# Performance work log

Hardware: AMD Instinct MI355X
Metric: run time of the kernel (lower is better)

The kernel has to match this reference:

```python
import jax, jax.numpy as jnp
import numpy as np

N_NODES = 100000
N_EDGES = 3200000
IN_CH = 128
HID = 64
OUT_CH = 2
BN_EPS = 1e-5


def setup_inputs() -> dict:
    key = jax.random.key(0)
    ks = jax.random.split(key, 16)
    def glorot(k, shape):
        fan_in, fan_out = shape[0], shape[1]
        lim = jnp.sqrt(6.0 / (fan_in + fan_out))
        return jax.random.uniform(k, shape, jnp.float32, -lim, lim)
    inp = {
        "x": jax.random.normal(ks[0], (N_NODES, IN_CH), jnp.float32),
        "edge_index": jax.random.randint(ks[1], (2, N_EDGES), 0, N_NODES, jnp.int64),
        # input projection + input BN
        "Wp": glorot(ks[2], (IN_CH, HID)),
        "bp": jnp.zeros((HID,), jnp.float32),
        "g_in": jnp.ones((HID,), jnp.float32),
        "b_in": jnp.zeros((HID,), jnp.float32),
        # SAGEConv layer 0: lin_l (aggr, with bias) + lin_r (self, no bias)
        "Wl0": glorot(ks[3], (HID, HID)),
        "bl0": jnp.zeros((HID,), jnp.float32),
        "Wr0": glorot(ks[4], (HID, HID)),
        "g0": jnp.ones((HID,), jnp.float32),
        "b0": jnp.zeros((HID,), jnp.float32),
        # SAGEConv layer 1
        "Wl1": glorot(ks[5], (HID, HID)),
        "bl1": jnp.zeros((HID,), jnp.float32),
        "Wr1": glorot(ks[6], (HID, HID)),
        "g1": jnp.ones((HID,), jnp.float32),
        "b1": jnp.zeros((HID,), jnp.float32),
        # output head
        "Wo": glorot(ks[7], (HID, OUT_CH)),
        "bo": jnp.zeros((OUT_CH,), jnp.float32),
    }
    return inp


def _bn(h, g, b):
    # training-mode batchnorm over node dim (biased variance, as torch)
    m = h.mean(axis=0)
    v = h.var(axis=0)
    return g * (h - m) * jax.lax.rsqrt(v + BN_EPS) + b


def _sage_conv(h, src, dst, Wl, bl, Wr):
    # mean aggregation of source features at destination nodes
    msg = h[src]                                              # [E, HID]
    summed = jax.ops.segment_sum(msg, dst, num_segments=N_NODES)
    cnt = jax.ops.segment_sum(jnp.ones((src.shape[0],), h.dtype), dst,
                              num_segments=N_NODES)
    aggr = summed / jnp.maximum(cnt, 1.0)[:, None]
    return aggr @ Wl + bl + h @ Wr


def reference(x, edge_index, Wp, bp, g_in, b_in,
              Wl0, bl0, Wr0, g0, b0,
              Wl1, bl1, Wr1, g1, b1,
              Wo, bo):
    src, dst = edge_index[0], edge_index[1]
    h = jax.nn.relu(_bn(x @ Wp + bp, g_in, b_in))   # dropout: eval no-op
    h_prev = h
    # layer 0 (i=0: no residual)
    h_new = jax.nn.relu(_bn(_sage_conv(h, src, dst, Wl0, bl0, Wr0), g0, b0))
    h_prev, h = h, h_new
    # layer 1 (i=1: residual with h_prev)
    h_new = jax.nn.relu(_bn(_sage_conv(h, src, dst, Wl1, bl1, Wr1), g1, b1))
    h_new = h_new + h_prev
    h = h_new
    return h @ Wo + bo
```

## Files before the change

### kernel.cpp

```cpp
#include <hip/hip_runtime.h>
#include <hip/hip_bf16.h>

#define NN 100000
#define NE 3200000
#define IC 128
#define HD 64
#define BN_EPS 1e-5f
#define NBUK 196
#define MSB 16
#define CAP 20480

__device__ __forceinline__ float bf2f(unsigned short u) {
  return __uint_as_float(((unsigned)u) << 16);
}
__device__ __forceinline__ unsigned int f2bf(float f) {
  unsigned int u = __float_as_uint(f);
  return (u + 0x7FFFu + ((u >> 16) & 1u)) >> 16;
}
__device__ __forceinline__ unsigned int pack2(float a, float b) {
  return f2bf(a) | (f2bf(b) << 16);
}

__global__ __launch_bounds__(256) void k_gemm_in(
    const float* __restrict__ x, const float* __restrict__ Wp,
    const float* __restrict__ bp, unsigned int* __restrict__ pre16,
    float* __restrict__ stats) {
  __shared__ float sW[IC * HD];
  __shared__ unsigned int sXu[64 * 68];
  __shared__ float sStS[256], sStQ[256];
  int tid = threadIdx.x;
  for (int i = tid; i < IC * HD / 4; i += 256)
    *(float4*)&sW[i * 4] = *(const float4*)&Wp[i * 4];
  int cg = tid & 15, rg = tid >> 4;
  int c0 = cg * 4;
  float4 bpc = *(const float4*)&bp[c0];
  float S[4] = {0.f, 0.f, 0.f, 0.f}, Q[4] = {0.f, 0.f, 0.f, 0.f};
  const int NT = (NN + 63) / 64;
  for (int t = blockIdx.x; t < NT; t += gridDim.x) {
    int row0 = t * 64;
    __syncthreads();
    for (int i = tid; i < 1024; i += 256) {
      int r = i >> 4, k8 = i & 15;
      int grow = row0 + r;
      if (grow >= NN) grow = NN - 1;
      const float* xs = &x[(size_t)grow * IC + k8 * 8];
      float4 f0 = *(const float4*)xs;
      float4 f1 = *(const float4*)(xs + 4);
      uint4 p;
      p.x = pack2(f0.x, f0.y);
      p.y = pack2(f0.z, f0.w);
      p.z = pack2(f1.x, f1.y);
      p.w = pack2(f1.z, f1.w);
      *(uint4*)&sXu[r * 68 + k8 * 4] = p;
    }
    __syncthreads();
    float acc[4][4];
#pragma unroll
    for (int r = 0; r < 4; ++r)
#pragma unroll
      for (int c = 0; c < 4; ++c) acc[r][c] = ((const float*)&bpc)[c];
    for (int kg = 0; kg < IC; kg += 4) {
      uint2 xu[4];
      float4 wv[4];
#pragma unroll
      for (int r = 0; r < 4; ++r)
        xu[r] = *(const uint2*)&sXu[(rg * 4 + r) * 68 + (kg >> 1)];
#pragma unroll
      for (int j = 0; j < 4; ++j)
        wv[j] = *(const float4*)&sW[(kg + j) * HD + c0];
#pragma unroll
      for (int r = 0; r < 4; ++r) {
        float xv[4];
        xv[0] = __uint_as_float(xu[r].x << 16);
        xv[1] = __uint_as_float(xu[r].x & 0xFFFF0000u);
        xv[2] = __uint_as_float(xu[r].y << 16);
        xv[3] = __uint_as_float(xu[r].y & 0xFFFF0000u);
#pragma unroll
        for (int j = 0; j < 4; ++j) {
#pragma unroll
          for (int c = 0; c < 4; ++c)
            acc[r][c] = fmaf(xv[j], ((const float*)&wv[j])[c], acc[r][c]);
        }
      }
    }
#pragma unroll
    for (int r = 0; r < 4; ++r) {
      int row = row0 + rg * 4 + r;
      if (row < NN) {
        uint2 o;
        o.x = pack2(acc[r][0], acc[r][1]);
        o.y = pack2(acc[r][2], acc[r][3]);
        *(uint2*)&pre16[(size_t)row * 32 + cg * 2] = o;
#pragma unroll
        for (int c = 0; c < 4; ++c) {
          S[c] += acc[r][c];
          Q[c] = fmaf(acc[r][c], acc[r][c], Q[c]);
        }
      }
    }
  }
#pragma unroll
  for (int c = 0; c < 4; ++c) {
    S[c] += __shfl_xor(S[c], 16);
    S[c] += __shfl_xor(S[c], 32);
    Q[c] += __shfl_xor(Q[c], 16);
    Q[c] += __shfl_xor(Q[c], 32);
  }
  int wave = tid >> 6, lane = tid & 63;
  if (lane < 16) {
#pragma unroll
    for (int c = 0; c < 4; ++c) {
      sStS[wave * 64 + lane * 4 + c] = S[c];
      sStQ[wave * 64 + lane * 4 + c] = Q[c];
    }
  }
  __syncthreads();
  if (tid < 64) {
    float Ts = sStS[tid] + sStS[64 + tid] + sStS[128 + tid] + sStS[192 + tid];
    float Tq = sStQ[tid] + sStQ[64 + tid] + sStQ[128 + tid] + sStQ[192 + tid];
    atomicAdd(&stats[tid], Ts);
    atomicAdd(&stats[64 + tid], Tq);
  }
}

__global__ __launch_bounds__(256) void k_bn_relu(
    const unsigned int* __restrict__ pre16, const float* __restrict__ stats,
    const float* __restrict__ g, const float* __restrict__ b,
    unsigned int* __restrict__ h16u) {
  size_t i = (size_t)blockIdx.x * 256 + threadIdx.x;
  int c0 = ((int)(i & 15)) * 4;
  const float invN = 1.0f / NN;
  uint2 p = *(const uint2*)&pre16[i * 2];
  float v[4];
  v[0] = __uint_as_float(p.x << 16);
  v[1] = __uint_as_float(p.x & 0xFFFF0000u);
  v[2] = __uint_as_float(p.y << 16);
  v[3] = __uint_as_float(p.y & 0xFFFF0000u);
#pragma unroll
  for (int c = 0; c < 4; ++c) {
    float m = stats[c0 + c] * invN;
    float var = stats[64 + c0 + c] * invN - m * m;
    float sc = g[c0 + c] * rsqrtf(var + BN_EPS);
    v[c] = fmaxf((v[c] - m) * sc + b[c0 + c], 0.f);
  }
  uint2 o;
  o.x = pack2(v[0], v[1]);
  o.y = pack2(v[2], v[3]);
  *(uint2*)&h16u[i * 2] = o;
}

__global__ __launch_bounds__(256) void k_initcur(unsigned int* __restrict__ gcur) {
  int t = threadIdx.x;
  if (t < NBUK) gcur[t] = (unsigned int)(t * CAP);
}

__global__ __launch_bounds__(256) void k_msplit(
    const int* __restrict__ src, const int* __restrict__ dst,
    unsigned int* __restrict__ gcur, unsigned int* __restrict__ staging) {
  __shared__ unsigned int hist[NBUK];
  __shared__ unsigned int gbase[NBUK];
  int tid = threadIdx.x;
  for (int i = tid; i < NBUK; i += 256) hist[i] = 0u;
  __syncthreads();
  int e0 = blockIdx.x * (256 * MSB);
  unsigned int pk[MSB], rk[MSB], bk[MSB];
#pragma unroll
  for (int i = 0; i < MSB; ++i) {
    int e = e0 + i * 256 + tid;
    if (e < NE) {
      int d = dst[e];
      unsigned int b = (unsigned int)(d >> 9);
      rk[i] = atomicAdd(&hist[b], 1u);
      pk[i] = (unsigned int)src[e] | ((unsigned int)(d & 511) << 17);
      bk[i] = b;
    } else {
      bk[i] = 0xFFFFFFFFu;
    }
  }
  __syncthreads();
  for (int i = tid; i < NBUK; i += 256)
    if (hist[i]) gbase[i] = atomicAdd(&gcur[i], hist[i]);
  __syncthreads();
#pragma unroll
  for (int i = 0; i < MSB; ++i)
    if (bk[i] != 0xFFFFFFFFu) staging[gbase[bk[i]] + rk[i]] = pk[i];
}

__global__ __launch_bounds__(256) void k_cscan(
    const unsigned int* __restrict__ gcur, unsigned int* __restrict__ gstart) {
  __shared__ unsigned int s[256];
  int t = threadIdx.x;
  unsigned int my = (t < NBUK) ? (gcur[t] - (unsigned int)(t * CAP)) : 0u;
  s[t] = my;
  __syncthreads();
  for (int off = 1; off < 256; off <<= 1) {
    unsigned int v = (t >= off) ? s[t - off] : 0u;
    __syncthreads();
    s[t] += v;
    __syncthreads();
  }
  if (t < NBUK) gstart[t] = s[t] - my;
  if (t == NBUK - 1) gstart[NBUK] = s[t];
}

__global__ __launch_bounds__(512) void k_bucket_sort(
    const unsigned int* __restrict__ staging,
    const unsigned int* __restrict__ gstart, unsigned int* __restrict__ nstart,
    unsigned int* __restrict__ srcoff) {
  __shared__ unsigned int hist[512];
  __shared__ unsigned int sc[512];
  __shared__ unsigned int cur[512];
  int b = blockIdx.x, t = threadIdx.x;
  hist[t] = 0u;
  __syncthreads();
  int base_in = b * CAP;
  int lo = (int)gstart[b];
  int cnt = (int)gstart[b + 1] - lo;
  for (int i = t; i < cnt; i += 512)
    atomicAdd(&hist[staging[base_in + i] >> 17], 1u);
  __syncthreads();
  unsigned int my = hist[t];
  sc[t] = my;
  __syncthreads();
  for (int off = 1; off < 512; off <<= 1) {
    unsigned int v = (t >= off) ? sc[t - off] : 0u;
    __syncthreads();
    sc[t] += v;
    __syncthreads();
  }
  unsigned int st = (unsigned int)lo + sc[t] - my;
  cur[t] = st;
  int node = b * 512 + t;
  if (node < NN) {
    nstart[node] = st;
    if (node == NN - 1) nstart[NN] = st + my;
  }
  __syncthreads();
  for (int i = t; i < cnt; i += 512) {
    unsigned int u = staging[base_in + i];
    unsigned int pos = atomicAdd(&cur[u >> 17], 1u);
    srcoff[pos] = (u & 0x1FFFFu) << 7;
  }
}

__global__ __launch_bounds__(256) void k_aggr_sorted(
    const unsigned int* __restrict__ srcoff,
    const unsigned int* __restrict__ nstart,
    const unsigned short* __restrict__ h16,
    unsigned short* __restrict__ a16) {
  int lane = threadIdx.x & 63;
  int n = (int)((blockIdx.x * 256 + threadIdx.x) >> 6);
  if (n >= NN) return;
  int g = lane >> 3;
  int q = lane & 7;
  int e0 = (int)nstart[n];
  int e1 = (int)nstart[n + 1];
  const char* hbase = (const char*)h16 + q * 16;
  float a0 = 0.f, a1 = 0.f, a2 = 0.f, a3 = 0.f;
  float a4 = 0.f, a5 = 0.f, a6 = 0.f, a7 = 0.f;
  float b0 = 0.f, b1 = 0.f, b2 = 0.f, b3 = 0.f;
  float b4 = 0.f, b5 = 0.f, b6 = 0.f, b7 = 0.f;
  int e = e0 + g;
  for (; e + 8 < e1; e += 16) {
    unsigned int o0 = srcoff[e];
    unsigned int o1 = srcoff[e + 8];
    uint4 u0 = *(const uint4*)(hbase + o0);
    uint4 u1 = *(const uint4*)(hbase + o1);
    a0 += __uint_as_float(u0.x << 16);
    a1 += __uint_as_float(u0.x & 0xFFFF0000u);
    a2 += __uint_as_float(u0.y << 16);
    a3 += __uint_as_float(u0.y & 0xFFFF0000u);
    a4 += __uint_as_float(u0.z << 16);
    a5 += __uint_as_float(u0.z & 0xFFFF0000u);
    a6 += __uint_as_float(u0.w << 16);
    a7 += __uint_as_float(u0.w & 0xFFFF0000u);
    b0 += __uint_as_float(u1.x << 16);
    b1 += __uint_as_float(u1.x & 0xFFFF0000u);
    b2 += __uint_as_float(u1.y << 16);
    b3 += __uint_as_float(u1.y & 0xFFFF0000u);
    b4 += __uint_as_float(u1.z << 16);
    b5 += __uint_as_float(u1.z & 0xFFFF0000u);
    b6 += __uint_as_float(u1.w << 16);
    b7 += __uint_as_float(u1.w & 0xFFFF0000u);
  }
  if (e < e1) {
    unsigned int o0 = srcoff[e];
    uint4 u0 = *(const uint4*)(hbase + o0);
    a0 += __uint_as_float(u0.x << 16);
    a1 += __uint_as_float(u0.x & 0xFFFF0000u);
    a2 += __uint_as_float(u0.y << 16);
    a3 += __uint_as_float(u0.y & 0xFFFF0000u);
    a4 += __uint_as_float(u0.z << 16);
    a5 += __uint_as_float(u0.z & 0xFFFF0000u);
    a6 += __uint_as_float(u0.w << 16);
    a7 += __uint_as_float(u0.w & 0xFFFF0000u);
  }
  a0 += b0; a1 += b1; a2 += b2; a3 += b3;
  a4 += b4; a5 += b5; a6 += b6; a7 += b7;
#pragma unroll
  for (int off = 8; off <= 32; off <<= 1) {
    a0 += __shfl_xor(a0, off);
    a1 += __shfl_xor(a1, off);
    a2 += __shfl_xor(a2, off);
    a3 += __shfl_xor(a3, off);
    a4 += __shfl_xor(a4, off);
    a5 += __shfl_xor(a5, off);
    a6 += __shfl_xor(a6, off);
    a7 += __shfl_xor(a7, off);
  }
  if (g == 0) {
    float cntf = (float)(e1 - e0);
    float inv = (cntf > 0.f) ? 1.0f / cntf : 0.f;
    uint4 o;
    o.x = pack2(a0 * inv, a1 * inv);
    o.y = pack2(a2 * inv, a3 * inv);
    o.z = pack2(a4 * inv, a5 * inv);
    o.w = pack2(a6 * inv, a7 * inv);
    *(uint4*)((char*)a16 + (size_t)n * 128 + q * 16) = o;
  }
}

__global__ __launch_bounds__(256) void k_combine(
    const unsigned int* __restrict__ a16u,
    const unsigned int* __restrict__ h16u, const float* __restrict__ Wl,
    const float* __restrict__ bl, const float* __restrict__ Wr,
    unsigned int* __restrict__ pre16, float* __restrict__ stats) {
  __shared__ float sWl[HD * HD], sWr[HD * HD];
  __shared__ unsigned int sAu[64 * 36], sHu[64 * 36];
  __shared__ float sStS[256], sStQ[256];
  int tid = threadIdx.x;
  for (int i = tid; i < HD * HD / 4; i += 256) {
    *(float4*)&sWl[i * 4] = *(const float4*)&Wl[i * 4];
    *(float4*)&sWr[i * 4] = *(const float4*)&Wr[i * 4];
  }
  int cg = tid & 15, rg = tid >> 4;
  int c0 = cg * 4;
  float4 blc = *(const float4*)&bl[c0];
  float S[4] = {0.f, 0.f, 0.f, 0.f}, Q[4] = {0.f, 0.f, 0.f, 0.f};
  const int NT = (NN + 63) / 64;
  for (int t = blockIdx.x; t < NT; t += gridDim.x) {
    int row0 = t * 64;
    __syncthreads();
    for (int i = tid; i < 512; i += 256) {
      int r = i >> 3, c4 = i & 7;
      int grow = row0 + r;
      if (grow >= NN) grow = NN - 1;
      *(uint4*)&sAu[r * 36 + c4 * 4] =
          *(const uint4*)&a16u[(size_t)grow * 32 + c4 * 4];
      *(uint4*)&sHu[r * 36 + c4 * 4] =
          *(const uint4*)&h16u[(size_t)grow * 32 + c4 * 4];
    }
    __syncthreads();
    float acc[4][4];
#pragma unroll
    for (int r = 0; r < 4; ++r)
#pragma unroll
      for (int c = 0; c < 4; ++c) acc[r][c] = ((const float*)&blc)[c];
    for (int kg = 0; kg < HD; kg += 4) {
      uint2 au[4], hu[4];
      float4 wlv[4], wrv[4];
#pragma unroll
      for (int r = 0; r < 4; ++r) {
        au[r] = *(const uint2*)&sAu[(rg * 4 + r) * 36 + (kg >> 1)];
        hu[r] = *(const uint2*)&sHu[(rg * 4 + r) * 36 + (kg >> 1)];
      }
#pragma unroll
      for (int j = 0; j < 4; ++j) {
        wlv[j] = *(const float4*)&sWl[(kg + j) * HD + c0];
        wrv[j] = *(const float4*)&sWr[(kg + j) * HD + c0];
      }
#pragma unroll
      for (int r = 0; r < 4; ++r) {
        float av[4], hv[4];
        av[0] = __uint_as_float(au[r].x << 16);
        av[1] = __uint_as_float(au[r].x & 0xFFFF0000u);
        av[2] = __uint_as_float(au[r].y << 16);
        av[3] = __uint_as_float(au[r].y & 0xFFFF0000u);
        hv[0] = __uint_as_float(hu[r].x << 16);
        hv[1] = __uint_as_float(hu[r].x & 0xFFFF0000u);
        hv[2] = __uint_as_float(hu[r].y << 16);
        hv[3] = __uint_as_float(hu[r].y & 0xFFFF0000u);
#pragma unroll
        for (int j = 0; j < 4; ++j) {
#pragma unroll
          for (int c = 0; c < 4; ++c) {
            acc[r][c] = fmaf(av[j], ((const float*)&wlv[j])[c], acc[r][c]);
            acc[r][c] = fmaf(hv[j], ((const float*)&wrv[j])[c], acc[r][c]);
          }
        }
      }
    }
#pragma unroll
    for (int r = 0; r < 4; ++r) {
      int row = row0 + rg * 4 + r;
      if (row < NN) {
        uint2 o;
        o.x = pack2(acc[r][0], acc[r][1]);
        o.y = pack2(acc[r][2], acc[r][3]);
        *(uint2*)&pre16[(size_t)row * 32 + cg * 2] = o;
#pragma unroll
        for (int c = 0; c < 4; ++c) {
          S[c] += acc[r][c];
          Q[c] = fmaf(acc[r][c], acc[r][c], Q[c]);
        }
      }
    }
  }
#pragma unroll
  for (int c = 0; c < 4; ++c) {
    S[c] += __shfl_xor(S[c], 16);
    S[c] += __shfl_xor(S[c], 32);
    Q[c] += __shfl_xor(Q[c], 16);
    Q[c] += __shfl_xor(Q[c], 32);
  }
  int wave = tid >> 6, lane = tid & 63;
  if (lane < 16) {
#pragma unroll
    for (int c = 0; c < 4; ++c) {
      sStS[wave * 64 + lane * 4 + c] = S[c];
      sStQ[wave * 64 + lane * 4 + c] = Q[c];
    }
  }
  __syncthreads();
  if (tid < 64) {
    float Ts = sStS[tid] + sStS[64 + tid] + sStS[128 + tid] + sStS[192 + tid];
    float Tq = sStQ[tid] + sStQ[64 + tid] + sStQ[128 + tid] + sStQ[192 + tid];
    atomicAdd(&stats[tid], Ts);
    atomicAdd(&stats[64 + tid], Tq);
  }
}

__global__ __launch_bounds__(256) void k_bn_relu_head(
    const unsigned short* __restrict__ pre16,
    const float* __restrict__ stats, const float* __restrict__ g,
    const float* __restrict__ b, const unsigned short* __restrict__ resid16,
    const float* __restrict__ Wo, const float* __restrict__ bo,
    float* __restrict__ out) {
  int lane = threadIdx.x & 63;
  int wid = (int)((blockIdx.x * blockDim.x + threadIdx.x) >> 6);
  int nw = (int)((gridDim.x * blockDim.x) >> 6);
  const float invN = 1.0f / NN;
  float m = stats[lane] * invN;
  float v = stats[64 + lane] * invN - m * m;
  float sc = g[lane] * rsqrtf(v + BN_EPS);
  float bb = b[lane];
  float w0 = Wo[lane * 2], w1 = Wo[lane * 2 + 1];
  float b0 = bo[0], b1 = bo[1];
  for (int row = wid; row < NN; row += nw) {
    size_t i = (size_t)row * HD + lane;
    float val = (bf2f(pre16[i]) - m) * sc + bb;
    val = fmaxf(val, 0.f) + bf2f(resid16[i]);
    float a0 = val * w0, a1 = val * w1;
#pragma unroll
    for (int off = 32; off > 0; off >>= 1) {
      a0 += __shfl_down(a0, off);
      a1 += __shfl_down(a1, off);
    }
    if (lane == 0) {
      out[(size_t)row * 2] = a0 + b0;
      out[(size_t)row * 2 + 1] = a1 + b1;
    }
  }
}

extern "C" void kernel_launch(void* const* d_in, const int* in_sizes, int n_in,
                              void* d_out, int out_size, void* d_ws,
                              size_t ws_size, hipStream_t stream) {
  const float* x = (const float*)d_in[0];
  const int* ei = (const int*)d_in[1];
  const float* Wp = (const float*)d_in[2];
  const float* bp = (const float*)d_in[3];
  const float* g_in = (const float*)d_in[4];
  const float* b_in = (const float*)d_in[5];
  const float* Wl0 = (const float*)d_in[6];
  const float* bl0 = (const float*)d_in[7];
  const float* Wr0 = (const float*)d_in[8];
  const float* g0 = (const float*)d_in[9];
  const float* b0 = (const float*)d_in[10];
  const float* Wl1 = (const float*)d_in[11];
  const float* bl1 = (const float*)d_in[12];
  const float* Wr1 = (const float*)d_in[13];
  const float* g1 = (const float*)d_in[14];
  const float* b1 = (const float*)d_in[15];
  const float* Wo = (const float*)d_in[16];
  const float* bo = (const float*)d_in[17];
  float* out = (float*)d_out;

  const int* src = ei;
  const int* dst = ei + NE;

  unsigned int* pre16 = (unsigned int*)d_ws;
  unsigned short* h0 = (unsigned short*)(pre16 + (size_t)NN * 32);
  unsigned short* h1 = h0 + (size_t)NN * HD;
  unsigned short* a16 = h1 + (size_t)NN * HD;
  unsigned int* staging = (unsigned int*)(a16 + (size_t)NN * HD);
  unsigned int* srcoff = staging + (size_t)NBUK * CAP;
  unsigned int* nstart = srcoff + NE;
  unsigned int* gstart = nstart + NN + 1;
  unsigned int* gcur = gstart + NBUK + 1;
  float* stats0 = (float*)(gcur + NBUK);
  float* stats1 = stats0 + 128;
  float* stats2 = stats1 + 128;

  const int BNR_BLOCKS = (NN * HD / 4) / 256;
  const int AGGR_BLOCKS = 25000;
  const int MS_BLOCKS = (NE + 256 * MSB - 1) / (256 * MSB);

  hipMemsetAsync(stats0, 0, 3 * 128 * sizeof(float), stream);

  k_gemm_in<<<768, 256, 0, stream>>>(x, Wp, bp, pre16, stats0);
  k_bn_relu<<<BNR_BLOCKS, 256, 0, stream>>>(pre16, stats0, g_in, b_in,
                                            (unsigned int*)h0);

  k_initcur<<<1, 256, 0, stream>>>(gcur);
  k_msplit<<<MS_BLOCKS, 256, 0, stream>>>(src, dst, gcur, staging);
  k_cscan<<<1, 256, 0, stream>>>(gcur, gstart);
  k_bucket_sort<<<NBUK, 512, 0, stream>>>(staging, gstart, nstart, srcoff);

  k_aggr_sorted<<<AGGR_BLOCKS, 256, 0, stream>>>(srcoff, nstart, h0, a16);
  k_combine<<<768, 256, 0, stream>>>((const unsigned int*)a16,
                                     (const unsigned int*)h0, Wl0, bl0, Wr0,
                                     pre16, stats1);
  k_bn_relu<<<BNR_BLOCKS, 256, 0, stream>>>(pre16, stats1, g0, b0,
                                            (unsigned int*)h1);

  k_aggr_sorted<<<AGGR_BLOCKS, 256, 0, stream>>>(srcoff, nstart, h1, a16);
  k_combine<<<768, 256, 0, stream>>>((const unsigned int*)a16,
                                     (const unsigned int*)h1, Wl1, bl1, Wr1,
                                     pre16, stats2);
  k_bn_relu_head<<<1024, 256, 0, stream>>>((const unsigned short*)pre16,
                                           stats2, g1, b1, h0, Wo, bo, out);
}
```

Baseline: 360.4 us.

## Use bf16 MFMA instructions for input projection and SAGE combine GEMMs

Replaces the scalar FMA register-tiled GEMMs in the input projection and the two combine kernels with 16x16x32 bf16 MFMA intrinsics. Weights are pre-packed into bf16 fragments in shared memory, and out-of-range rows are zero-filled instead of clamped. The aim is to cut the ALU cost of the dense matmuls. In exchange, output stores become scattered 2-byte writes per lane instead of packed 8-byte writes, and weights are now rounded to bf16, which loses some precision.

```diff
diff --git a/kernel.cpp b/kernel.cpp
--- a/kernel.cpp
+++ b/kernel.cpp
@@ -10,6 +10,9 @@
 #define MSB 16
 #define CAP 20480
 
+typedef __attribute__((ext_vector_type(8))) short bf16x8;
+typedef __attribute__((ext_vector_type(4))) float f32x4;
+
 __device__ __forceinline__ float bf2f(unsigned short u) {
   return __uint_as_float(((unsigned)u) << 16);
 }
@@ -23,17 +26,27 @@
 
 __global__ __launch_bounds__(256) void k_gemm_in(
     const float* __restrict__ x, const float* __restrict__ Wp,
-    const float* __restrict__ bp, unsigned int* __restrict__ pre16,
+    const float* __restrict__ bp, unsigned short* __restrict__ pre16,
     float* __restrict__ stats) {
-  __shared__ float sW[IC * HD];
   __shared__ unsigned int sXu[64 * 68];
+  __shared__ uint4 sWb[16 * 64];
   __shared__ float sStS[256], sStQ[256];
   int tid = threadIdx.x;
-  for (int i = tid; i < IC * HD / 4; i += 256)
-    *(float4*)&sW[i * 4] = *(const float4*)&Wp[i * 4];
-  int cg = tid & 15, rg = tid >> 4;
-  int c0 = cg * 4;
-  float4 bpc = *(const float4*)&bp[c0];
+  int wave = tid >> 6, lane = tid & 63;
+  int lm = lane & 15, lb = lane >> 4;
+  for (int i = tid; i < 1024; i += 256) {
+    int b = i >> 6, n = i & 63;
+    const float* wp = &Wp[(size_t)(8 * b) * HD + n];
+    uint4 p;
+    p.x = pack2(wp[0], wp[HD]);
+    p.y = pack2(wp[2 * HD], wp[3 * HD]);
+    p.z = pack2(wp[4 * HD], wp[5 * HD]);
+    p.w = pack2(wp[6 * HD], wp[7 * HD]);
+    sWb[i] = p;
+  }
+  float bias[4];
+#pragma unroll
+  for (int nt = 0; nt < 4; ++nt) bias[nt] = bp[nt * 16 + lm];
   float S[4] = {0.f, 0.f, 0.f, 0.f}, Q[4] = {0.f, 0.f, 0.f, 0.f};
   const int NT = (NN + 63) / 64;
   for (int t = blockIdx.x; t < NT; t += gridDim.x) {
@@ -42,76 +55,63 @@
     for (int i = tid; i < 1024; i += 256) {
       int r = i >> 4, k8 = i & 15;
       int grow = row0 + r;
-      if (grow >= NN) grow = NN - 1;
-      const float* xs = &x[(size_t)grow * IC + k8 * 8];
-      float4 f0 = *(const float4*)xs;
-      float4 f1 = *(const float4*)(xs + 4);
       uint4 p;
-      p.x = pack2(f0.x, f0.y);
-      p.y = pack2(f0.z, f0.w);
-      p.z = pack2(f1.x, f1.y);
-      p.w = pack2(f1.z, f1.w);
+      if (grow < NN) {
+        const float* xs = &x[(size_t)grow * IC + k8 * 8];
+        float4 f0 = *(const float4*)xs;
+        float4 f1 = *(const float4*)(xs + 4);
+        p.x = pack2(f0.x, f0.y);
+        p.y = pack2(f0.z, f0.w);
+        p.z = pack2(f1.x, f1.y);
+        p.w = pack2(f1.z, f1.w);
+      } else {
+        p.x = p.y = p.z = p.w = 0u;
+      }
       *(uint4*)&sXu[r * 68 + k8 * 4] = p;
     }
     __syncthreads();
-    float acc[4][4];
-#pragma unroll
-    for (int r = 0; r < 4; ++r)
-#pragma unroll
-      for (int c = 0; c < 4; ++c) acc[r][c] = ((const float*)&bpc)[c];
-    for (int kg = 0; kg < IC; kg += 4) {
-      uint2 xu[4];
-      float4 wv[4];
-#pragma unroll
-      for (int r = 0; r < 4; ++r)
-        xu[r] = *(const uint2*)&sXu[(rg * 4 + r) * 68 + (kg >> 1)];
-#pragma unroll
-      for (int j = 0; j < 4; ++j)
-        wv[j] = *(const float4*)&sW[(kg + j) * HD + c0];
+    f32x4 acc[4];
+#pragma unroll
+    for (int nt = 0; nt < 4; ++nt) acc[nt] = (f32x4){0.f, 0.f, 0.f, 0.f};
+#pragma unroll
+    for (int ks = 0; ks < 4; ++ks) {
+      bf16x8 af =
+          *(const bf16x8*)&sXu[(wave * 16 + lm) * 68 + ks * 16 + lb * 4];
+      int b = ks * 4 + lb;
+#pragma unroll
+      for (int nt = 0; nt < 4; ++nt) {
+        bf16x8 bf = *(const bf16x8*)&sWb[b * 64 + nt * 16 + lm];
+        acc[nt] = __builtin_amdgcn_mfma_f32_16x16x32_bf16(af, bf, acc[nt],
+                                                          0, 0, 0);
+      }
+    }
+    int rowl = wave * 16 + lb * 4;
+#pragma unroll
+    for (int nt = 0; nt < 4; ++nt) {
 #pragma unroll
       for (int r = 0; r < 4; ++r) {
-        float xv[4];
-        xv[0] = __uint_as_float(xu[r].x << 16);
-        xv[1] = __uint_as_float(xu[r].x & 0xFFFF0000u);
-        xv[2] = __uint_as_float(xu[r].y << 16);
-        xv[3] = __uint_as_float(xu[r].y & 0xFFFF0000u);
-#pragma unroll
-        for (int j = 0; j < 4; ++j) {
-#pragma unroll
-          for (int c = 0; c < 4; ++c)
-            acc[r][c] = fmaf(xv[j], ((const float*)&wv[j])[c], acc[r][c]);
+        int grow = row0 + rowl + r;
+        if (grow < NN) {
+          float val = acc[nt][r] + bias[nt];
+          pre16[(size_t)grow * HD + nt * 16 + lm] = (unsigned short)f2bf(val);
+          S[nt] += val;
+          Q[nt] = fmaf(val, val, Q[nt]);
         }
       }
     }
-#pragma unroll
-    for (int r = 0; r < 4; ++r) {
-      int row = row0 + rg * 4 + r;
-      if (row < NN) {
-        uint2 o;
-        o.x = pack2(acc[r][0], acc[r][1]);
-        o.y = pack2(acc[r][2], acc[r][3]);
-        *(uint2*)&pre16[(size_t)row * 32 + cg * 2] = o;
-#pragma unroll
-        for (int c = 0; c < 4; ++c) {
-          S[c] += acc[r][c];
-          Q[c] = fmaf(acc[r][c], acc[r][c], Q[c]);
-        }
-      }
-    }
-  }
-#pragma unroll
-  for (int c = 0; c < 4; ++c) {
-    S[c] += __shfl_xor(S[c], 16);
-    S[c] += __shfl_xor(S[c], 32);
-    Q[c] += __shfl_xor(Q[c], 16);
-    Q[c] += __shfl_xor(Q[c], 32);
-  }
-  int wave = tid >> 6, lane = tid & 63;
+  }
+#pragma unroll
+  for (int nt = 0; nt < 4; ++nt) {
+    S[nt] += __shfl_xor(S[nt], 16);
+    S[nt] += __shfl_xor(S[nt], 32);
+    Q[nt] += __shfl_xor(Q[nt], 16);
+    Q[nt] += __shfl_xor(Q[nt], 32);
+  }
   if (lane < 16) {
 #pragma unroll
-    for (int c = 0; c < 4; ++c) {
-      sStS[wave * 64 + lane * 4 + c] = S[c];
-      sStQ[wave * 64 + lane * 4 + c] = Q[c];
+    for (int nt = 0; nt < 4; ++nt) {
+      sStS[wave * 64 + nt * 16 + lane] = S[nt];
+      sStQ[wave * 64 + nt * 16 + lane] = Q[nt];
     }
   }
   __syncthreads();
@@ -324,18 +324,27 @@
     const unsigned int* __restrict__ a16u,
     const unsigned int* __restrict__ h16u, const float* __restrict__ Wl,
     const float* __restrict__ bl, const float* __restrict__ Wr,
-    unsigned int* __restrict__ pre16, float* __restrict__ stats) {
-  __shared__ float sWl[HD * HD], sWr[HD * HD];
+    unsigned short* __restrict__ pre16, float* __restrict__ stats) {
   __shared__ unsigned int sAu[64 * 36], sHu[64 * 36];
+  __shared__ uint4 sWb[2 * 8 * 64];
   __shared__ float sStS[256], sStQ[256];
   int tid = threadIdx.x;
-  for (int i = tid; i < HD * HD / 4; i += 256) {
-    *(float4*)&sWl[i * 4] = *(const float4*)&Wl[i * 4];
-    *(float4*)&sWr[i * 4] = *(const float4*)&Wr[i * 4];
-  }
-  int cg = tid & 15, rg = tid >> 4;
-  int c0 = cg * 4;
-  float4 blc = *(const float4*)&bl[c0];
+  int wave = tid >> 6, lane = tid & 63;
+  int lm = lane & 15, lb = lane >> 4;
+  for (int i = tid; i < 1024; i += 256) {
+    int m = i >> 9, rem = i & 511;
+    int b = rem >> 6, n = rem & 63;
+    const float* w = (m == 0 ? Wl : Wr) + (size_t)(8 * b) * HD + n;
+    uint4 p;
+    p.x = pack2(w[0], w[HD]);
+    p.y = pack2(w[2 * HD], w[3 * HD]);
+    p.z = pack2(w[4 * HD], w[5 * HD]);
+    p.w = pack2(w[6 * HD], w[7 * HD]);
+    sWb[i] = p;
+  }
+  float bias[4];
+#pragma unroll
+  for (int nt = 0; nt < 4; ++nt) bias[nt] = bl[nt * 16 + lm];
   float S[4] = {0.f, 0.f, 0.f, 0.f}, Q[4] = {0.f, 0.f, 0.f, 0.f};
   const int NT = (NN + 63) / 64;
   for (int t = blockIdx.x; t < NT; t += gridDim.x) {
@@ -344,81 +353,65 @@
     for (int i = tid; i < 512; i += 256) {
       int r = i >> 3, c4 = i & 7;
       int grow = row0 + r;
-      if (grow >= NN) grow = NN - 1;
-      *(uint4*)&sAu[r * 36 + c4 * 4] =
-          *(const uint4*)&a16u[(size_t)grow * 32 + c4 * 4];
-      *(uint4*)&sHu[r * 36 + c4 * 4] =
-          *(const uint4*)&h16u[(size_t)grow * 32 + c4 * 4];
-    }
-    __syncthreads();
-    float acc[4][4];
-#pragma unroll
-    for (int r = 0; r < 4; ++r)
-#pragma unroll
-      for (int c = 0; c < 4; ++c) acc[r][c] = ((const float*)&blc)[c];
-    for (int kg = 0; kg < HD; kg += 4) {
-      uint2 au[4], hu[4];
-      float4 wlv[4], wrv[4];
+      uint4 pa, ph;
+      if (grow < NN) {
+        pa = *(const uint4*)&a16u[(size_t)grow * 32 + c4 * 4];
+        ph = *(const uint4*)&h16u[(size_t)grow * 32 + c4 * 4];
+      } else {
+        pa.x = pa.y = pa.z = pa.w = 0u;
+        ph = pa;
+      }
+      *(uint4*)&sAu[r * 36 + c4 * 4] = pa;
+      *(uint4*)&sHu[r * 36 + c4 * 4] = ph;
+    }
+    __syncthreads();
+    f32x4 acc[4];
+#pragma unroll
+    for (int nt = 0; nt < 4; ++nt) acc[nt] = (f32x4){0.f, 0.f, 0.f, 0.f};
+#pragma unroll
+    for (int ks = 0; ks < 2; ++ks) {
+      bf16x8 af =
+          *(const bf16x8*)&sAu[(wave * 16 + lm) * 36 + ks * 16 + lb * 4];
+      bf16x8 hf =
+          *(const bf16x8*)&sHu[(wave * 16 + lm) * 36 + ks * 16 + lb * 4];
+      int b = ks * 4 + lb;
+#pragma unroll
+      for (int nt = 0; nt < 4; ++nt) {
+        bf16x8 wlf = *(const bf16x8*)&sWb[b * 64 + nt * 16 + lm];
+        bf16x8 wrf = *(const bf16x8*)&sWb[512 + b * 64 + nt * 16 + lm];
+        acc[nt] = __builtin_amdgcn_mfma_f32_16x16x32_bf16(af, wlf, acc[nt],
+                                                          0, 0, 0);
+        acc[nt] = __builtin_amdgcn_mfma_f32_16x16x32_bf16(hf, wrf, acc[nt],
+                                                          0, 0, 0);
+      }
+    }
+    int rowl = wave * 16 + lb * 4;
+#pragma unroll
+    for (int nt = 0; nt < 4; ++nt) {
 #pragma unroll
       for (int r = 0; r < 4; ++r) {
-        au[r] = *(const uint2*)&sAu[(rg * 4 + r) * 36 + (kg >> 1)];
-        hu[r] = *(const uint2*)&sHu[(rg * 4 + r) * 36 + (kg >> 1)];
-      }
-#pragma unroll
-      for (int j = 0; j < 4; ++j) {
-        wlv[j] = *(const float4*)&sWl[(kg + j) * HD + c0];
-        wrv[j] = *(const float4*)&sWr[(kg + j) * HD + c0];
-      }
-#pragma unroll
-      for (int r = 0; r < 4; ++r) {
-        float av[4], hv[4];
-        av[0] = __uint_as_float(au[r].x << 16);
-        av[1] = __uint_as_float(au[r].x & 0xFFFF0000u);
-        av[2] = __uint_as_float(au[r].y << 16);
-        av[3] = __uint_as_float(au[r].y & 0xFFFF0000u);
-        hv[0] = __uint_as_float(hu[r].x << 16);
-        hv[1] = __uint_as_float(hu[r].x & 0xFFFF0000u);
-        hv[2] = __uint_as_float(hu[r].y << 16);
-        hv[3] = __uint_as_float(hu[r].y & 0xFFFF0000u);
-#pragma unroll
-        for (int j = 0; j < 4; ++j) {
-#pragma unroll
-          for (int c = 0; c < 4; ++c) {
-            acc[r][c] = fmaf(av[j], ((const float*)&wlv[j])[c], acc[r][c]);
-            acc[r][c] = fmaf(hv[j], ((const float*)&wrv[j])[c], acc[r][c]);
-          }
+        int grow = row0 + rowl + r;
+        if (grow < NN) {
+          float val = acc[nt][r] + bias[nt];
+          pre16[(size_t)grow * HD + nt * 16 + lm] = (unsigned short)f2bf(val);
+          S[nt] += val;
+          Q[nt] = fmaf(val, val, Q[nt]);
         }
       }
     }
-#pragma unroll
-    for (int r = 0; r < 4; ++r) {
-      int row = row0 + rg * 4 + r;
-      if (row < NN) {
-        uint2 o;
-        o.x = pack2(acc[r][0], acc[r][1]);
-        o.y = pack2(acc[r][2], acc[r][3]);
-        *(uint2*)&pre16[(size_t)row * 32 + cg * 2] = o;
-#pragma unroll
-        for (int c = 0; c < 4; ++c) {
-          S[c] += acc[r][c];
-          Q[c] = fmaf(acc[r][c], acc[r][c], Q[c]);
-        }
-      }
-    }
-  }
-#pragma unroll
-  for (int c = 0; c < 4; ++c) {
-    S[c] += __shfl_xor(S[c], 16);
-    S[c] += __shfl_xor(S[c], 32);
-    Q[c] += __shfl_xor(Q[c], 16);
-    Q[c] += __shfl_xor(Q[c], 32);
-  }
-  int wave = tid >> 6, lane = tid & 63;
+  }
+#pragma unroll
+  for (int nt = 0; nt < 4; ++nt) {
+    S[nt] += __shfl_xor(S[nt], 16);
+    S[nt] += __shfl_xor(S[nt], 32);
+    Q[nt] += __shfl_xor(Q[nt], 16);
+    Q[nt] += __shfl_xor(Q[nt], 32);
+  }
   if (lane < 16) {
 #pragma unroll
-    for (int c = 0; c < 4; ++c) {
-      sStS[wave * 64 + lane * 4 + c] = S[c];
-      sStQ[wave * 64 + lane * 4 + c] = Q[c];
+    for (int nt = 0; nt < 4; ++nt) {
+      sStS[wave * 64 + nt * 16 + lane] = S[nt];
+      sStQ[wave * 64 + nt * 16 + lane] = Q[nt];
     }
   }
   __syncthreads();
@@ -508,7 +501,8 @@
 
   hipMemsetAsync(stats0, 0, 3 * 128 * sizeof(float), stream);
 
-  k_gemm_in<<<768, 256, 0, stream>>>(x, Wp, bp, pre16, stats0);
+  k_gemm_in<<<768, 256, 0, stream>>>(x, Wp, bp, (unsigned short*)pre16,
+                                     stats0);
   k_bn_relu<<<BNR_BLOCKS, 256, 0, stream>>>(pre16, stats0, g_in, b_in,
                                             (unsigned int*)h0);
 
@@ -520,14 +514,14 @@
   k_aggr_sorted<<<AGGR_BLOCKS, 256, 0, stream>>>(srcoff, nstart, h0, a16);
   k_combine<<<768, 256, 0, stream>>>((const unsigned int*)a16,
                                      (const unsigned int*)h0, Wl0, bl0, Wr0,
-                                     pre16, stats1);
+                                     (unsigned short*)pre16, stats1);
   k_bn_relu<<<BNR_BLOCKS, 256, 0, stream>>>(pre16, stats1, g0, b0,
                                             (unsigned int*)h1);
 
   k_aggr_sorted<<<AGGR_BLOCKS, 256, 0, stream>>>(srcoff, nstart, h1, a16);
   k_combine<<<768, 256, 0, stream>>>((const unsigned int*)a16,
                                      (const unsigned int*)h1, Wl1, bl1, Wr1,
-                                     pre16, stats2);
+                                     (unsigned short*)pre16, stats2);
   k_bn_relu_head<<<1024, 256, 0, stream>>>((const unsigned short*)pre16,
                                            stats2, g1, b1, h0, Wo, bo, out);
 }
```

Measured after the change: 340.0 us. -5.7%, faster.
